# Kernel optimization log

Hardware: AMD Instinct MI355X
Metric: run time of the kernel (lower is better)

## Reference

```python
import jax, jax.numpy as jnp
import numpy as np

EPS = 1e-5

def _bn(h, gamma, beta):
    # BatchNorm1d in training mode: per-channel stats over the batch dim (L=1)
    m = jnp.mean(h, axis=0)
    v = jnp.var(h, axis=0)  # biased variance, as torch uses for normalization
    return gamma * (h - m) * jax.lax.rsqrt(v + EPS) + beta

def setup_inputs() -> dict:
    key = jax.random.key(0)
    ks = jax.random.split(key, 8)
    vocab, emb = 8192, 512
    inter = (vocab + emb) // 2  # 4352
    N = 8192
    x_t = jax.random.randint(ks[0], (N,), 0, vocab, dtype=jnp.int64)
    W1 = jax.random.normal(ks[1], (inter, vocab), dtype=jnp.float32) * 0.02
    b1 = jax.random.normal(ks[2], (inter,), dtype=jnp.float32) * 0.02
    g1 = jnp.ones((inter,), dtype=jnp.float32)
    beta1 = jnp.zeros((inter,), dtype=jnp.float32)
    W2 = jax.random.normal(ks[3], (emb, inter), dtype=jnp.float32) * 0.02
    b2 = jax.random.normal(ks[4], (emb,), dtype=jnp.float32) * 0.02
    g2 = jnp.ones((emb,), dtype=jnp.float32)
    beta2 = jnp.zeros((emb,), dtype=jnp.float32)
    return {"x_t": x_t, "W1": W1, "b1": b1, "g1": g1, "beta1": beta1,
            "W2": W2, "b2": b2, "g2": g2, "beta2": beta2}

def reference(x_t, W1, b1, g1, beta1, W2, b2, g2, beta2):
    # one_hot(x_t) @ Conv1d(k=1) weight == gather of W1 columns (same math, no dense one-hot)
    h1 = W1.T[x_t] + b1                      # [N, inter]
    h1 = jax.nn.gelu(_bn(h1, g1, beta1), approximate=False)
    h2 = h1 @ W2.T + b2                      # [N, emb]
    out = jax.nn.gelu(_bn(h2, g2, beta2), approximate=False)
    return out
```

## Files before the change

kernel.cpp:

```cpp
#include <hip/hip_runtime.h>
#include <hip/hip_bf16.h>
#include <math.h>

typedef __attribute__((ext_vector_type(8))) short short8;
typedef __attribute__((ext_vector_type(4))) float f32x4;

#define VOCAB 8192
#define NSAMP 8192
#define INTER 4352
#define EMB   512

#define OFF_CNT    0
#define OFF_A1     32768
#define OFF_M1     50176
#define OFF_A2     67584
#define OFF_M2     69632
#define OFF_PS1B   71680
#define OFF_PS2B   1120256
#define OFF_W2B    2168832
#define OFF_HACT   6625280
#define OFF_H2     77928448

__device__ __forceinline__ float gelu_exact(float x) {
    return 0.5f * x * (1.0f + erff(x * 0.70710678118654752f));
}
__device__ __forceinline__ unsigned short f2bf(float x) {
    __hip_bfloat16 b = __float2bfloat16(x);
    return *reinterpret_cast<unsigned short*>(&b);
}
__device__ __forceinline__ void async16(const unsigned short* g, unsigned short* l) {
    __builtin_amdgcn_global_load_lds(
        (const __attribute__((address_space(1))) void*)g,
        (__attribute__((address_space(3))) void*)l, 16, 0, 0);
}

__global__ void k_zero_cnt(int* cnt) {
    cnt[blockIdx.x * 256 + threadIdx.x] = 0;
}
__global__ void k_hist(const int* __restrict__ xt, int* __restrict__ cnt) {
    int n = blockIdx.x * 256 + threadIdx.x;
    atomicAdd(&cnt[xt[n]], 1);
}

__global__ __launch_bounds__(256) void k_stats1(const float* __restrict__ W1,
                                                const int* __restrict__ cnt,
                                                const float* __restrict__ g1,
                                                float* __restrict__ a1,
                                                float* __restrict__ m1) {
    const int t = threadIdx.x, lane = t & 63, w = t >> 6;
    const int row = blockIdx.x * 4 + w;
    const float* wr = W1 + (size_t)row * VOCAB;
    float s1 = 0.f, s2 = 0.f;
    #pragma unroll 8
    for (int it = 0; it < 32; ++it) {
        int v = it * 256 + lane * 4;
        float4 x = *(const float4*)(wr + v);
        int4 c = *(const int4*)(cnt + v);
        float cx = (float)c.x, cy = (float)c.y, cz = (float)c.z, cw = (float)c.w;
        s1 += cx * x.x + cy * x.y + cz * x.z + cw * x.w;
        s2 += cx * x.x * x.x + cy * x.y * x.y + cz * x.z * x.z + cw * x.w * x.w;
    }
    #pragma unroll
    for (int d = 1; d < 64; d <<= 1) {
        s1 += __shfl_xor(s1, d);
        s2 += __shfl_xor(s2, d);
    }
    if (lane == 0) {
        float m = s1 * (1.f / NSAMP);
        float var = s2 * (1.f / NSAMP) - m * m;
        a1[row] = g1[row] * rsqrtf(var + 1e-5f);
        m1[row] = m;
    }
}

__global__ __launch_bounds__(256) void k_build(const float* __restrict__ W1,
                                               const float* __restrict__ a1,
                                               const float* __restrict__ m1,
                                               const float* __restrict__ beta1,
                                               unsigned short* __restrict__ Hact) {
    const int i0 = blockIdx.x * 64;
    const int v0 = blockIdx.y * 256;
    const int t = threadIdx.x;
    const int c0 = (t & 15) * 4;
    const int vg = (t >> 4) * 4;
    float4 av = *(const float4*)(a1 + i0 + c0);
    float4 mv = *(const float4*)(m1 + i0 + c0);
    float4 bv = *(const float4*)(beta1 + i0 + c0);
    const float* ap = (const float*)&av;
    const float* mp = (const float*)&mv;
    const float* bp = (const float*)&bv;
    #pragma unroll
    for (int vi = 0; vi < 4; ++vi) {
        int vb = v0 + vi * 64 + vg;
        float wf[4][4];
        #pragma unroll
        for (int j = 0; j < 4; ++j)
            *(float4*)&wf[j][0] = *(const float4*)(W1 + (size_t)(i0 + c0 + j) * VOCAB + vb);
        #pragma unroll
        for (int k = 0; k < 4; ++k) {
            ushort4 o;
            o.x = f2bf(gelu_exact(ap[0] * (wf[0][k] - mp[0]) + bp[0]));
            o.y = f2bf(gelu_exact(ap[1] * (wf[1][k] - mp[1]) + bp[1]));
            o.z = f2bf(gelu_exact(ap[2] * (wf[2][k] - mp[2]) + bp[2]));
            o.w = f2bf(gelu_exact(ap[3] * (wf[3][k] - mp[3]) + bp[3]));
            *(ushort4*)&Hact[(size_t)(vb + k) * INTER + i0 + c0] = o;
        }
    }
}

__global__ void k_w2bf(const float* __restrict__ W2, unsigned short* __restrict__ W2b) {
    int idx = (blockIdx.x * 256 + threadIdx.x) * 4;
    float4 w = *(const float4*)(W2 + idx);
    ushort4 u;
    u.x = f2bf(w.x); u.y = f2bf(w.y); u.z = f2bf(w.z); u.w = f2bf(w.w);
    *(ushort4*)(W2b + idx) = u;
}

__global__ __launch_bounds__(512) void k_gemm(const unsigned short* __restrict__ A,
                                              const unsigned short* __restrict__ B,
                                              const int* __restrict__ cnt,
                                              float* __restrict__ h2,
                                              float* __restrict__ ps1,
                                              float* __restrict__ ps2) {
    __shared__ __align__(16) unsigned short sA[2][128 * 64];
    __shared__ __align__(16) unsigned short sB[2][128 * 64];
    const int bid = blockIdx.x;
    const int mblk = bid >> 2;
    const int nblk = bid & 3;
    const int m0 = mblk * 128;
    const int n0 = nblk * 128;
    const int t = threadIdx.x;
    const int lane = t & 63;
    const int wave = t >> 6;
    const int wr = wave >> 2, wc = wave & 3;
    const int mq = lane & 15, kq = lane >> 4;
    const int srow = lane >> 3;
    const int sgrp = lane & 7;
    const int scol = (sgrp ^ srow) * 8;
    const int swz = mq & 7;

    const unsigned short* Ab = A + (size_t)(m0 + wave * 16 + srow) * INTER + scol;
    const unsigned short* Bb = B + (size_t)(n0 + wave * 16 + srow) * INTER + scol;

    f32x4 acc[4][2];
    #pragma unroll
    for (int r = 0; r < 4; ++r)
        #pragma unroll
        for (int c = 0; c < 2; ++c) acc[r][c] = (f32x4){0.f, 0.f, 0.f, 0.f};

    auto stage = [&](int buf, int k0) {
        async16(Ab + k0,                         &sA[buf][(wave * 16) * 64]);
        async16(Ab + (size_t)8 * INTER + k0,     &sA[buf][(wave * 16 + 8) * 64]);
        async16(Bb + k0,                         &sB[buf][(wave * 16) * 64]);
        async16(Bb + (size_t)8 * INTER + k0,     &sB[buf][(wave * 16 + 8) * 64]);
    };
    auto compute = [&](int buf) {
        #pragma unroll
        for (int kk = 0; kk < 64; kk += 32) {
            const int gbase = kq + (kk >> 3);
            short8 af[4], bfr[2];
            #pragma unroll
            for (int r = 0; r < 4; ++r)
                af[r] = *(const short8*)&sA[buf][(wr * 64 + r * 16 + mq) * 64 + ((gbase ^ swz) * 8)];
            #pragma unroll
            for (int c = 0; c < 2; ++c)
                bfr[c] = *(const short8*)&sB[buf][(wc * 32 + c * 16 + mq) * 64 + ((gbase ^ swz) * 8)];
            #pragma unroll
            for (int r = 0; r < 4; ++r)
                #pragma unroll
                for (int c = 0; c < 2; ++c)
                    acc[r][c] = __builtin_amdgcn_mfma_f32_16x16x32_bf16(af[r], bfr[c], acc[r][c], 0, 0, 0);
        }
    };

    stage(0, 0);
    __syncthreads();
    for (int ti = 0; ti < 67; ++ti) {
        stage((ti + 1) & 1, (ti + 1) * 64);
        compute(ti & 1);
        __syncthreads();
    }
    compute(1);

    float s1[2] = {0.f, 0.f}, s2[2] = {0.f, 0.f};
    #pragma unroll
    for (int r = 0; r < 4; ++r) {
        const int rowb = m0 + wr * 64 + r * 16 + kq * 4;
        int4 cw = *(const int4*)(cnt + rowb);
        float w0 = (float)cw.x, w1 = (float)cw.y, w2 = (float)cw.z, w3 = (float)cw.w;
        #pragma unroll
        for (int c = 0; c < 2; ++c) {
            const int col = n0 + wc * 32 + c * 16 + mq;
            float v0 = acc[r][c][0], v1 = acc[r][c][1], v2 = acc[r][c][2], v3 = acc[r][c][3];
            h2[(size_t)(rowb + 0) * EMB + col] = v0;
            h2[(size_t)(rowb + 1) * EMB + col] = v1;
            h2[(size_t)(rowb + 2) * EMB + col] = v2;
            h2[(size_t)(rowb + 3) * EMB + col] = v3;
            s1[c] += w0 * v0 + w1 * v1 + w2 * v2 + w3 * v3;
            s2[c] += w0 * v0 * v0 + w1 * v1 * v1 + w2 * v2 * v2 + w3 * v3 * v3;
        }
    }
    #pragma unroll
    for (int c = 0; c < 2; ++c) {
        s1[c] += __shfl_xor(s1[c], 16);
        s2[c] += __shfl_xor(s2[c], 16);
        s1[c] += __shfl_xor(s1[c], 32);
        s2[c] += __shfl_xor(s2[c], 32);
    }
    if (lane < 16) {
        const int slot = mblk * 2 + wr;
        #pragma unroll
        for (int c = 0; c < 2; ++c) {
            const int col = n0 + wc * 32 + c * 16 + mq;
            ps1[(size_t)col * 128 + slot] = s1[c];
            ps2[(size_t)col * 128 + slot] = s2[c];
        }
    }
}

__global__ __launch_bounds__(256) void k_stats2f(const float* __restrict__ ps1,
                                                 const float* __restrict__ ps2,
                                                 const float* __restrict__ g2,
                                                 float* __restrict__ a2,
                                                 float* __restrict__ m2) {
    const int lane = threadIdx.x & 63;
    const int e = blockIdx.x * 4 + (threadIdx.x >> 6);
    float s1 = ps1[(size_t)e * 128 + lane] + ps1[(size_t)e * 128 + 64 + lane];
    float s2 = ps2[(size_t)e * 128 + lane] + ps2[(size_t)e * 128 + 64 + lane];
    #pragma unroll
    for (int d = 1; d < 64; d <<= 1) {
        s1 += __shfl_xor(s1, d);
        s2 += __shfl_xor(s2, d);
    }
    if (lane == 0) {
        float m = s1 * (1.f / NSAMP);
        float var = s2 * (1.f / NSAMP) - m * m;
        a2[e] = g2[e] * rsqrtf(var + 1e-5f);
        m2[e] = m;
    }
}

__global__ __launch_bounds__(256) void k_final(const float* __restrict__ h2,
                                               const int* __restrict__ xt,
                                               const float* __restrict__ a2,
                                               const float* __restrict__ m2,
                                               const float* __restrict__ beta2,
                                               float* __restrict__ out) {
    const int t = threadIdx.x;
    const int n = blockIdx.x * 2 + (t >> 7);
    const int e = (t & 127) * 4;
    const int v = xt[n];
    float4 h = *(const float4*)(h2 + (size_t)v * EMB + e);
    float4 a = *(const float4*)(a2 + e);
    float4 m = *(const float4*)(m2 + e);
    float4 b = *(const float4*)(beta2 + e);
    float4 o;
    o.x = gelu_exact(a.x * (h.x - m.x) + b.x);
    o.y = gelu_exact(a.y * (h.y - m.y) + b.y);
    o.z = gelu_exact(a.z * (h.z - m.z) + b.z);
    o.w = gelu_exact(a.w * (h.w - m.w) + b.w);
    *(float4*)(out + (size_t)n * EMB + e) = o;
}

extern "C" void kernel_launch(void* const* d_in, const int* in_sizes, int n_in,
                              void* d_out, int out_size, void* d_ws, size_t ws_size,
                              hipStream_t stream) {
    const int* xt      = (const int*)d_in[0];
    const float* W1    = (const float*)d_in[1];
    const float* g1    = (const float*)d_in[3];
    const float* beta1 = (const float*)d_in[4];
    const float* W2    = (const float*)d_in[5];
    const float* g2    = (const float*)d_in[7];
    const float* beta2 = (const float*)d_in[8];
    float* out = (float*)d_out;

    char* ws = (char*)d_ws;
    int*   cnt  = (int*)  (ws + OFF_CNT);
    float* a1   = (float*)(ws + OFF_A1);
    float* m1   = (float*)(ws + OFF_M1);
    float* a2   = (float*)(ws + OFF_A2);
    float* m2   = (float*)(ws + OFF_M2);
    float* ps1b = (float*)(ws + OFF_PS1B);
    float* ps2b = (float*)(ws + OFF_PS2B);
    unsigned short* W2b  = (unsigned short*)(ws + OFF_W2B);
    unsigned short* Hact = (unsigned short*)(ws + OFF_HACT);
    float* h2   = (float*)(ws + OFF_H2);

    k_zero_cnt<<<32, 256, 0, stream>>>(cnt);
    k_hist<<<32, 256, 0, stream>>>(xt, cnt);
    k_stats1<<<1088, 256, 0, stream>>>(W1, cnt, g1, a1, m1);
    k_build<<<dim3(68, 32), 256, 0, stream>>>(W1, a1, m1, beta1, Hact);
    k_w2bf<<<2176, 256, 0, stream>>>(W2, W2b);
    k_gemm<<<256, 512, 0, stream>>>(Hact, W2b, cnt, h2, ps1b, ps2b);
    k_stats2f<<<128, 256, 0, stream>>>(ps1b, ps2b, g2, a2, m2);
    k_final<<<4096, 256, 0, stream>>>(h2, xt, a2, m2, beta2, out);
}
```

Before: 344.1 us.

## Fuse small kernels, deepen GEMM LDS pipeline to four stages, fold BN2 stats into GEMM

Replaces the zero and histogram kernels with one single-block LDS histogram, and merges the W2 bf16 conversion into the Hact build kernel as extra blocks. The GEMM moves from a double-buffered to a four-stage LDS ring with explicit vmcnt waits and raised MFMA priority. A last-block-done atomic counter lets the final GEMM block reduce the BN2 partial sums, which removes the separate stats kernel. Together these cut launch overhead and aim to hide global-load latency, at the cost of more LDS per block (possible occupancy loss) and a serial tail reduction in one block.

```diff
diff --git a/kernel.cpp b/kernel.cpp
--- a/kernel.cpp
+++ b/kernel.cpp
@@ -16,6 +16,7 @@
 #define OFF_A2     67584
 #define OFF_M2     69632
 #define OFF_PS1B   71680
+#define OFF_DONE   333824
 #define OFF_PS2B   1120256
 #define OFF_W2B    2168832
 #define OFF_HACT   6625280
@@ -34,12 +35,25 @@
         (__attribute__((address_space(3))) void*)l, 16, 0, 0);
 }
 
-__global__ void k_zero_cnt(int* cnt) {
-    cnt[blockIdx.x * 256 + threadIdx.x] = 0;
-}
-__global__ void k_hist(const int* __restrict__ xt, int* __restrict__ cnt) {
-    int n = blockIdx.x * 256 + threadIdx.x;
-    atomicAdd(&cnt[xt[n]], 1);
+__global__ __launch_bounds__(1024) void k_hist1b(const int* __restrict__ xt,
+                                                 int* __restrict__ cnt,
+                                                 unsigned* __restrict__ done) {
+    __shared__ int h[VOCAB];
+    const int t = threadIdx.x;
+    #pragma unroll
+    for (int i = 0; i < 8; ++i) h[t + i * 1024] = 0;
+    if (t == 0) *done = 0u;
+    __syncthreads();
+    const int4* x4 = (const int4*)xt;
+    int4 a = x4[t], b = x4[t + 1024];
+    atomicAdd(&h[a.x], 1); atomicAdd(&h[a.y], 1);
+    atomicAdd(&h[a.z], 1); atomicAdd(&h[a.w], 1);
+    atomicAdd(&h[b.x], 1); atomicAdd(&h[b.y], 1);
+    atomicAdd(&h[b.z], 1); atomicAdd(&h[b.w], 1);
+    __syncthreads();
+    #pragma unroll
+    for (int i = 0; i < 2; ++i)
+        ((int4*)cnt)[t + i * 1024] = ((const int4*)h)[t + i * 1024];
 }
 
 __global__ __launch_bounds__(256) void k_stats1(const float* __restrict__ W1,
@@ -73,14 +87,25 @@
     }
 }
 
-__global__ __launch_bounds__(256) void k_build(const float* __restrict__ W1,
-                                               const float* __restrict__ a1,
-                                               const float* __restrict__ m1,
-                                               const float* __restrict__ beta1,
-                                               unsigned short* __restrict__ Hact) {
-    const int i0 = blockIdx.x * 64;
-    const int v0 = blockIdx.y * 256;
+__global__ __launch_bounds__(256) void k_buildw2(const float* __restrict__ W1,
+                                                 const float* __restrict__ a1,
+                                                 const float* __restrict__ m1,
+                                                 const float* __restrict__ beta1,
+                                                 unsigned short* __restrict__ Hact,
+                                                 const float* __restrict__ W2,
+                                                 unsigned short* __restrict__ W2b) {
+    const int bx = blockIdx.x;
     const int t = threadIdx.x;
+    if (bx >= 2176) {
+        int idx = ((bx - 2176) * 256 + t) * 4;
+        float4 w = *(const float4*)(W2 + idx);
+        ushort4 u;
+        u.x = f2bf(w.x); u.y = f2bf(w.y); u.z = f2bf(w.z); u.w = f2bf(w.w);
+        *(ushort4*)(W2b + idx) = u;
+        return;
+    }
+    const int i0 = (bx % 68) * 64;
+    const int v0 = (bx / 68) * 256;
     const int c0 = (t & 15) * 4;
     const int vg = (t >> 4) * 4;
     float4 av = *(const float4*)(a1 + i0 + c0);
@@ -108,22 +133,18 @@
     }
 }
 
-__global__ void k_w2bf(const float* __restrict__ W2, unsigned short* __restrict__ W2b) {
-    int idx = (blockIdx.x * 256 + threadIdx.x) * 4;
-    float4 w = *(const float4*)(W2 + idx);
-    ushort4 u;
-    u.x = f2bf(w.x); u.y = f2bf(w.y); u.z = f2bf(w.z); u.w = f2bf(w.w);
-    *(ushort4*)(W2b + idx) = u;
-}
-
 __global__ __launch_bounds__(512) void k_gemm(const unsigned short* __restrict__ A,
                                               const unsigned short* __restrict__ B,
                                               const int* __restrict__ cnt,
                                               float* __restrict__ h2,
                                               float* __restrict__ ps1,
-                                              float* __restrict__ ps2) {
-    __shared__ __align__(16) unsigned short sA[2][128 * 64];
-    __shared__ __align__(16) unsigned short sB[2][128 * 64];
+                                              float* __restrict__ ps2,
+                                              const float* __restrict__ g2,
+                                              float* __restrict__ a2,
+                                              float* __restrict__ m2,
+                                              unsigned* __restrict__ done) {
+    __shared__ __align__(16) unsigned short sA[4][128 * 64];
+    __shared__ __align__(16) unsigned short sB[4][128 * 64];
     const int bid = blockIdx.x;
     const int mblk = bid >> 2;
     const int nblk = bid & 3;
@@ -148,11 +169,12 @@
         #pragma unroll
         for (int c = 0; c < 2; ++c) acc[r][c] = (f32x4){0.f, 0.f, 0.f, 0.f};
 
-    auto stage = [&](int buf, int k0) {
-        async16(Ab + k0,                         &sA[buf][(wave * 16) * 64]);
-        async16(Ab + (size_t)8 * INTER + k0,     &sA[buf][(wave * 16 + 8) * 64]);
-        async16(Bb + k0,                         &sB[buf][(wave * 16) * 64]);
-        async16(Bb + (size_t)8 * INTER + k0,     &sB[buf][(wave * 16 + 8) * 64]);
+    auto stage = [&](int buf, int tile) {
+        int k0 = tile * 64;
+        async16(Ab + k0,                     &sA[buf][(wave * 16) * 64]);
+        async16(Ab + (size_t)8 * INTER + k0, &sA[buf][(wave * 16 + 8) * 64]);
+        async16(Bb + k0,                     &sB[buf][(wave * 16) * 64]);
+        async16(Bb + (size_t)8 * INTER + k0, &sB[buf][(wave * 16 + 8) * 64]);
     };
     auto compute = [&](int buf) {
         #pragma unroll
@@ -165,22 +187,39 @@
             #pragma unroll
             for (int c = 0; c < 2; ++c)
                 bfr[c] = *(const short8*)&sB[buf][(wc * 32 + c * 16 + mq) * 64 + ((gbase ^ swz) * 8)];
+            __builtin_amdgcn_s_setprio(1);
             #pragma unroll
             for (int r = 0; r < 4; ++r)
                 #pragma unroll
                 for (int c = 0; c < 2; ++c)
                     acc[r][c] = __builtin_amdgcn_mfma_f32_16x16x32_bf16(af[r], bfr[c], acc[r][c], 0, 0, 0);
+            __builtin_amdgcn_s_setprio(0);
         }
     };
 
-    stage(0, 0);
-    __syncthreads();
-    for (int ti = 0; ti < 67; ++ti) {
-        stage((ti + 1) & 1, (ti + 1) * 64);
-        compute(ti & 1);
-        __syncthreads();
-    }
-    compute(1);
+#define PSTEP(BUF, VM, STG, TILE3)                                 \
+    {                                                              \
+        asm volatile("s_waitcnt vmcnt(" #VM ")" ::: "memory");     \
+        __builtin_amdgcn_sched_barrier(0);                         \
+        __builtin_amdgcn_s_barrier();                              \
+        __builtin_amdgcn_sched_barrier(0);                         \
+        if (STG) stage(((BUF) + 3) & 3, TILE3);                    \
+        compute(BUF);                                              \
+    }
+
+    stage(0, 0); stage(1, 1); stage(2, 2);
+    #pragma unroll 1
+    for (int tt = 0; tt < 64; tt += 4) {
+        PSTEP(0, 8, 1, tt + 3)
+        PSTEP(1, 8, 1, tt + 4)
+        PSTEP(2, 8, 1, tt + 5)
+        PSTEP(3, 8, 1, tt + 6)
+    }
+    PSTEP(0, 8, 1, 67)
+    PSTEP(1, 8, 0, 0)
+    PSTEP(2, 4, 0, 0)
+    PSTEP(3, 0, 0, 0)
+#undef PSTEP
 
     float s1[2] = {0.f, 0.f}, s2[2] = {0.f, 0.f};
     #pragma unroll
@@ -216,27 +255,28 @@
             ps2[(size_t)col * 128 + slot] = s2[c];
         }
     }
-}
-
-__global__ __launch_bounds__(256) void k_stats2f(const float* __restrict__ ps1,
-                                                 const float* __restrict__ ps2,
-                                                 const float* __restrict__ g2,
-                                                 float* __restrict__ a2,
-                                                 float* __restrict__ m2) {
-    const int lane = threadIdx.x & 63;
-    const int e = blockIdx.x * 4 + (threadIdx.x >> 6);
-    float s1 = ps1[(size_t)e * 128 + lane] + ps1[(size_t)e * 128 + 64 + lane];
-    float s2 = ps2[(size_t)e * 128 + lane] + ps2[(size_t)e * 128 + 64 + lane];
-    #pragma unroll
-    for (int d = 1; d < 64; d <<= 1) {
-        s1 += __shfl_xor(s1, d);
-        s2 += __shfl_xor(s2, d);
-    }
-    if (lane == 0) {
-        float m = s1 * (1.f / NSAMP);
-        float var = s2 * (1.f / NSAMP) - m * m;
-        a2[e] = g2[e] * rsqrtf(var + 1e-5f);
-        m2[e] = m;
+
+    __shared__ bool sLast;
+    __syncthreads();
+    if (t == 0) {
+        __threadfence();
+        sLast = (atomicAdd(done, 1u) == 255u);
+    }
+    __syncthreads();
+    if (sLast) {
+        __threadfence();
+        float f1 = 0.f, f2 = 0.f;
+        const float4* p1 = (const float4*)(ps1 + (size_t)t * 128);
+        const float4* p2 = (const float4*)(ps2 + (size_t)t * 128);
+        #pragma unroll 8
+        for (int i = 0; i < 32; ++i) {
+            float4 u = p1[i]; f1 += u.x + u.y + u.z + u.w;
+            float4 v = p2[i]; f2 += v.x + v.y + v.z + v.w;
+        }
+        float m = f1 * (1.f / NSAMP);
+        float var = f2 * (1.f / NSAMP) - m * m;
+        a2[t] = g2[t] * rsqrtf(var + 1e-5f);
+        m2[t] = m;
     }
 }
 
@@ -282,16 +322,14 @@
     float* m2   = (float*)(ws + OFF_M2);
     float* ps1b = (float*)(ws + OFF_PS1B);
     float* ps2b = (float*)(ws + OFF_PS2B);
+    unsigned* done = (unsigned*)(ws + OFF_DONE);
     unsigned short* W2b  = (unsigned short*)(ws + OFF_W2B);
     unsigned short* Hact = (unsigned short*)(ws + OFF_HACT);
     float* h2   = (float*)(ws + OFF_H2);
 
-    k_zero_cnt<<<32, 256, 0, stream>>>(cnt);
-    k_hist<<<32, 256, 0, stream>>>(xt, cnt);
+    k_hist1b<<<1, 1024, 0, stream>>>(xt, cnt, done);
     k_stats1<<<1088, 256, 0, stream>>>(W1, cnt, g1, a1, m1);
-    k_build<<<dim3(68, 32), 256, 0, stream>>>(W1, a1, m1, beta1, Hact);
-    k_w2bf<<<2176, 256, 0, stream>>>(W2, W2b);
-    k_gemm<<<256, 512, 0, stream>>>(Hact, W2b, cnt, h2, ps1b, ps2b);
-    k_stats2f<<<128, 256, 0, stream>>>(ps1b, ps2b, g2, a2, m2);
+    k_buildw2<<<4352, 256, 0, stream>>>(W1, a1, m1, beta1, Hact, W2, W2b);
+    k_gemm<<<256, 512, 0, stream>>>(Hact, W2b, cnt, h2, ps1b, ps2b, g2, a2, m2, done);
     k_final<<<4096, 256, 0, stream>>>(h2, xt, a2, m2, beta2, out);
 }
```

Result: slower. 357.1 us (+3.8%).
